# Kernel tuning notes

Hardware: AMD Instinct MI355X
Metric: run time of the kernel (lower is better)

The kernel has to match this reference:

```python
import jax, jax.numpy as jnp
import numpy as np

SEQ, BS, H, D = 2048, 2, 16, 64


def phi(x):
    # ELU(x / d**0.25) + 1
    return jax.nn.elu(x / (x.shape[-1] ** 0.25)) + 1.0


def setup_inputs() -> dict:
    key = jax.random.key(0)
    ks = jax.random.split(key, 5)
    return {
        "query_layer": jax.random.normal(ks[0], (SEQ, BS, H, D), jnp.float32),
        "key_layer": jax.random.normal(ks[1], (SEQ, BS, H, D), jnp.float32),
        "value_layer": jax.random.normal(ks[2], (SEQ, BS, H, D), jnp.float32),
        "attention_mask": jnp.zeros((BS, 1, SEQ, SEQ), dtype=bool),  # unused by forward
        "phi_k": jax.random.normal(ks[3], (1, H, D, 1), jnp.float32) / 10000.0,
        "phi_kv": jax.random.normal(ks[4], (1, H, D, D), jnp.float32) / 10000.0,
    }


def _ntk_attn(q, k, v, sum_phi_k, sum_phi_kv):
    # q,k,v: [bs,h,n,d]; sum_phi_k: [1,h,d,1]; sum_phi_kv: [1,h,d,d]
    d = q.shape[-1]
    nq, nk = q.shape[-2], k.shape[-2]
    kk = jnp.abs(sum_phi_k)
    Z = sum_phi_kv
    phi_q = phi(q)  # [bs,h,nq,d]
    A = jnp.einsum("bhqd,bhkd->bhqk", q, k) / jnp.sqrt(jnp.float32(d))
    max_A = jnp.max(A, axis=-1, keepdims=True)  # [bs,h,nq,1]
    exp_max_A = jnp.exp(max_A)
    A = jnp.exp(A - max_A)
    causal = jnp.tril(jnp.ones((nq, nk), jnp.float32), k=nk - nq)
    A = A * causal  # broadcast over [bs,h]
    D_norm = jnp.sum(A, axis=-1, keepdims=True) + jnp.matmul(phi_q, kk) / exp_max_A
    ctx = (jnp.matmul(A, v) + jnp.matmul(phi_q, Z) / exp_max_A) / D_norm
    return ctx  # [bs,h,nq,d]


def reference(query_layer, key_layer, value_layer, attention_mask, phi_k, phi_kv):
    # inputs are [seq, bs, h, d]; attention_mask is unused (module ignores it)
    q = jnp.transpose(query_layer, (1, 2, 0, 3)).astype(jnp.float32)
    k = jnp.transpose(key_layer, (1, 2, 0, 3)).astype(jnp.float32)
    v = jnp.transpose(value_layer, (1, 2, 0, 3)).astype(jnp.float32)
    ctx = _ntk_attn(q, k, v, phi_k, phi_kv)  # [bs,h,nq,d]
    ctx = jnp.transpose(ctx, (2, 0, 1, 3))  # [nq,bs,h,d]
    nq, bs, h, d = ctx.shape
    return ctx.reshape(nq, bs, h * d).astype(query_layer.dtype)
```

## Files before the change

### kernel.cpp

```cpp
#include <hip/hip_runtime.h>

#define SEQ 2048
#define BSZ 2
#define NHEAD 16
#define NBH (BSZ * NHEAD)
#define HDIM 64
#define QBLK 64
#define KVBLK 64
#define NQT (SEQ / QBLK)
#define ROWSTRIDE (BSZ * NHEAD * HDIM)

typedef __bf16 bf16x8 __attribute__((ext_vector_type(8)));
typedef __bf16 bf16x4 __attribute__((ext_vector_type(4)));
typedef float f32x4 __attribute__((ext_vector_type(4)));

#define AS1 __attribute__((address_space(1)))
#define AS3 __attribute__((address_space(3)))

__global__ __launch_bounds__(256)
void conv_k(const float* __restrict__ Kg, __bf16* __restrict__ Kb) {
  const int t = blockIdx.x * 256 + threadIdx.x;
  const int s = t >> 8;
  const int bh = (t >> 3) & 31;
  const int d8 = (t & 7) * 8;
  const float* src = Kg + (size_t)s * ROWSTRIDE + bh * HDIM + d8;
  const float4 a = *(const float4*)src;
  const float4 b = *(const float4*)(src + 4);
  bf16x8 o = {(__bf16)a.x, (__bf16)a.y, (__bf16)a.z, (__bf16)a.w,
              (__bf16)b.x, (__bf16)b.y, (__bf16)b.z, (__bf16)b.w};
  const int slot = (d8 >> 3) ^ (s & 7);
  *(bf16x8*)(Kb + ((size_t)bh * SEQ + s) * HDIM + slot * 8) = o;
}

__global__ __launch_bounds__(256)
void conv_v(const float* __restrict__ Vg, __bf16* __restrict__ Vt) {
  __shared__ __bf16 tt[HDIM][72];
  const int kb = blockIdx.x;
  const int bh = blockIdx.y;
  const int tid = threadIdx.x;
  {
    const int r = tid >> 2, c16 = (tid & 3) * 16;
#pragma unroll
    for (int i = 0; i < 4; ++i) {
      const float4 v = *(const float4*)(Vg + (size_t)(kb * 64 + r) * ROWSTRIDE +
                                        bh * HDIM + c16 + 4 * i);
      tt[c16 + 4 * i + 0][r] = (__bf16)v.x;
      tt[c16 + 4 * i + 1][r] = (__bf16)v.y;
      tt[c16 + 4 * i + 2][r] = (__bf16)v.z;
      tt[c16 + 4 * i + 3][r] = (__bf16)v.w;
    }
  }
  __syncthreads();
  {
    const int d = tid >> 2, c2 = (tid & 3) * 2;
#pragma unroll
    for (int k8 = 0; k8 < 2; ++k8) {
      const int s8 = c2 + k8;
      const int pbase = (s8 ^ (d & 7)) * 8;
      __bf16 ov[8];
#pragma unroll
      for (int j = 0; j < 8; ++j) {
        const int p = pbase + j;
        const int P = p >> 5, g = (p >> 3) & 3, jj = p & 7;
        ov[j] = tt[d][32 * P + 16 * (jj >> 2) + 4 * g + (jj & 3)];
      }
      *(bf16x8*)(Vt + (((size_t)bh * 32 + kb) * 64 + d) * 64 + s8 * 8) =
          *(const bf16x8*)ov;
    }
  }
}

__global__ __launch_bounds__(256)
void conv_z(const float* __restrict__ PKVg, __bf16* __restrict__ Ztb) {
  const int t = blockIdx.x * 256 + threadIdx.x;
  const int lr = t & 15, lg = (t >> 4) & 3, c = (t >> 6) & 1;
  const int dj = (t >> 7) & 3, h = t >> 9;
  __bf16 o[8];
#pragma unroll
  for (int i = 0; i < 8; ++i)
    o[i] = (__bf16)PKVg[((size_t)h * 64 + 32 * c + 8 * lg + i) * 64 + dj * 16 + lr];
  *(bf16x8*)(Ztb + (size_t)t * 8) = *(const bf16x8*)o;
}

__global__ __launch_bounds__(256, 4)
void ntk_attn(const float* __restrict__ Qg, const __bf16* __restrict__ Kb,
              const __bf16* __restrict__ Vt, const float* __restrict__ PKg,
              const __bf16* __restrict__ Ztb, float* __restrict__ Og) {
  __shared__ __bf16 Ks[2][KVBLK * HDIM];
  __shared__ __bf16 Vts[2][KVBLK * HDIM];

  const int tid = threadIdx.x;
  const int w = tid >> 6, l = tid & 63, lr = l & 15, lg = l >> 4;

  const int ord = blockIdx.x;
  const int bh = ord & 31, h = bh & (NHEAD - 1);
  const int v = ord >> 5;
  const int bx = (v < 16) ? v : 47 - v;
  const int q0 = bx * QBLK;
  const int ntile = bx + 1;
  const int headoff = bh * HDIM;
  const __bf16* Kbh = Kb + (size_t)bh * SEQ * HDIM;
  const __bf16* Vbh = Vt + (size_t)bh * SEQ * HDIM;

  auto stage = [&](int kb, int bb) {
    const char* gk = (const char*)Kbh + ((size_t)kb << 13) + (w << 11) + (l << 4);
    const char* gv = (const char*)Vbh + ((size_t)kb << 13) + (w << 11) + (l << 4);
    __bf16* lk = &Ks[bb][w << 10];
    __bf16* lv = &Vts[bb][w << 10];
    __builtin_amdgcn_global_load_lds((const AS1 unsigned*)gk,
                                     (AS3 unsigned*)lk, 16, 0, 0);
    __builtin_amdgcn_global_load_lds((const AS1 unsigned*)(gk + 1024),
                                     (AS3 unsigned*)(lk + 512), 16, 0, 0);
    __builtin_amdgcn_global_load_lds((const AS1 unsigned*)gv,
                                     (AS3 unsigned*)lv, 16, 0, 0);
    __builtin_amdgcn_global_load_lds((const AS1 unsigned*)(gv + 1024),
                                     (AS3 unsigned*)(lv + 512), 16, 0, 0);
  };

  stage(0, 0);

  bf16x8 aq[2], pq[2];
  {
    const float* qp = Qg + (size_t)(q0 + w * 16 + lr) * ROWSTRIDE + headoff + lg * 8;
#pragma unroll
    for (int c = 0; c < 2; ++c) {
      const float4 x0 = *(const float4*)(qp + 32 * c);
      const float4 x1 = *(const float4*)(qp + 32 * c + 4);
      const float f[8] = {x0.x, x0.y, x0.z, x0.w, x1.x, x1.y, x1.z, x1.w};
#pragma unroll
      for (int i = 0; i < 8; ++i) {
        aq[c][i] = (__bf16)(f[i] * 0.125f);
        const float xs = f[i] * 0.3535533905932738f;
        pq[c][i] = (__bf16)(xs > 0.f ? xs + 1.f : __expf(xs));
      }
    }
  }

  const f32x4 z4 = {0.f, 0.f, 0.f, 0.f};
  f32x4 oacc[4] = {z4, z4, z4, z4};
  float lsum = 0.f;
  const int qa = q0 + w * 16 + lr;
  const int sw = lr & 7;

  __syncthreads();
  int cur = 0;

  for (int kb = 0; kb < ntile; ++kb) {
    const bool more = (kb + 1 < ntile);
    if (more) stage(kb + 1, cur ^ 1);

    bf16x8 kc[4][2];
#pragma unroll
    for (int nj = 0; nj < 4; ++nj)
#pragma unroll
      for (int c = 0; c < 2; ++c)
        kc[nj][c] = *(const bf16x8*)&Ks[cur][(nj * 16 + lr) * 64 +
                                            (((4 * c + lg) ^ sw) << 3)];
    bf16x8 vv[2][4];
#pragma unroll
    for (int P = 0; P < 2; ++P)
#pragma unroll
      for (int dj = 0; dj < 4; ++dj)
        vv[P][dj] = *(const bf16x8*)&Vts[cur][(dj * 16 + lr) * 64 +
                                             (((4 * P + lg) ^ sw) << 3)];

    f32x4 s4[4];
    __builtin_amdgcn_s_setprio(1);
#pragma unroll
    for (int nj = 0; nj < 4; ++nj) {
      f32x4 acc = z4;
#pragma unroll
      for (int c = 0; c < 2; ++c)
        acc = __builtin_amdgcn_mfma_f32_16x16x32_bf16(kc[nj][c], aq[c], acc, 0, 0, 0);
      s4[nj] = acc;
    }
    __builtin_amdgcn_s_setprio(0);

    bf16x4 p4[4];
    const bool diag = (kb == bx);
    const int kv0 = kb * KVBLK;
#pragma unroll
    for (int nj = 0; nj < 4; ++nj) {
#pragma unroll
      for (int r = 0; r < 4; ++r) {
        float e;
        if (diag) {
          const int kabs = kv0 + 16 * nj + 4 * lg + r;
          e = (kabs <= qa) ? __expf(s4[nj][r]) : 0.f;
        } else {
          e = __expf(s4[nj][r]);
        }
        lsum += e;
        p4[nj][r] = (__bf16)e;
      }
    }

    __builtin_amdgcn_s_setprio(1);
#pragma unroll
    for (int P = 0; P < 2; ++P) {
      const bf16x8 pa = __builtin_shufflevector(p4[2 * P], p4[2 * P + 1],
                                                0, 1, 2, 3, 4, 5, 6, 7);
#pragma unroll
      for (int dj = 0; dj < 4; ++dj)
        oacc[dj] = __builtin_amdgcn_mfma_f32_16x16x32_bf16(pa, vv[P][dj],
                                                           oacc[dj], 0, 0, 0);
    }
    __builtin_amdgcn_s_setprio(0);

    if (more) {
      __syncthreads();
      cur ^= 1;
    }
  }

  float den;
  {
    float pkk = 0.f;
#pragma unroll
    for (int c = 0; c < 2; ++c) {
      const float* kp = PKg + h * HDIM + 32 * c + 8 * lg;
      const float4 a = *(const float4*)kp;
      const float4 b = *(const float4*)(kp + 4);
      const float ka[8] = {a.x, a.y, a.z, a.w, b.x, b.y, b.z, b.w};
#pragma unroll
      for (int i = 0; i < 8; ++i)
        pkk += (float)pq[c][i] * fabsf(ka[i]);
    }
    pkk += __shfl_xor(pkk, 16);
    pkk += __shfl_xor(pkk, 32);
    float s = lsum;
    s += __shfl_xor(s, 16);
    s += __shfl_xor(s, 32);
    den = s + pkk;
  }

  f32x4 zacc[4] = {z4, z4, z4, z4};
  const __bf16* Zf = Ztb + (size_t)h * 4096;
  __builtin_amdgcn_s_setprio(1);
#pragma unroll
  for (int c = 0; c < 2; ++c) {
#pragma unroll
    for (int dj = 0; dj < 4; ++dj) {
      const bf16x8 bz = *(const bf16x8*)(Zf + ((dj * 2 + c) * 64 + l) * 8);
      zacc[dj] = __builtin_amdgcn_mfma_f32_16x16x32_bf16(pq[c], bz, zacc[dj], 0, 0, 0);
    }
  }
  __builtin_amdgcn_s_setprio(0);

#pragma unroll
  for (int r = 0; r < 4; ++r) {
    const float rd = 1.f / __shfl(den, lg * 4 + r);
    float* op = Og + (size_t)(q0 + w * 16 + lg * 4 + r) * ROWSTRIDE + headoff;
#pragma unroll
    for (int dj = 0; dj < 4; ++dj)
      op[dj * 16 + lr] = (oacc[dj][r] + zacc[dj][r]) * rd;
  }
}

extern "C" void kernel_launch(void* const* d_in, const int* in_sizes, int n_in,
                              void* d_out, int out_size, void* d_ws, size_t ws_size,
                              hipStream_t stream) {
  const float* Qg  = (const float*)d_in[0];
  const float* Kg  = (const float*)d_in[1];
  const float* Vg  = (const float*)d_in[2];
  const float* PKg  = (const float*)d_in[4];
  const float* PKVg = (const float*)d_in[5];
  float* Og = (float*)d_out;

  __bf16* Kb  = (__bf16*)d_ws;
  __bf16* Vt  = Kb + (size_t)NBH * SEQ * HDIM;
  __bf16* Ztb = Vt + (size_t)NBH * SEQ * HDIM;

  conv_k<<<dim3(SEQ * NBH * 8 / 256), dim3(256), 0, stream>>>(Kg, Kb);
  conv_v<<<dim3(SEQ / 64, NBH), dim3(256), 0, stream>>>(Vg, Vt);
  conv_z<<<dim3(32), dim3(256), 0, stream>>>(PKVg, Ztb);
  ntk_attn<<<dim3(NQT * NBH), dim3(256), 0, stream>>>(Qg, Kb, Vt, PKg, Ztb, Og);
}
```

Measured before the change: 53.00 us.

## Share K/V tiles across 128-row query blocks, fuse conversion kernels, use exp2

The attention kernel now processes 128 query rows per block with 512 threads, so each staged K/V tile in LDS serves twice as many query rows and global K/V traffic per query row is halved. Waves in the lower half skip the final K tile, which lies entirely above their causal diagonal. The three bf16 conversion kernels are merged into one launch that dispatches on block index, cutting launch overhead. The softmax exponent uses the hardware exp2 with log2(e) folded into the Q scale. In exchange the grid has half as many blocks, which lowers occupancy and parallelism, and some waves sit idle on the last tile.

```diff
diff --git a/kernel.cpp b/kernel.cpp
--- a/kernel.cpp
+++ b/kernel.cpp
@@ -5,7 +5,7 @@
 #define NHEAD 16
 #define NBH (BSZ * NHEAD)
 #define HDIM 64
-#define QBLK 64
+#define QBLK 128
 #define KVBLK 64
 #define NQT (SEQ / QBLK)
 #define ROWSTRIDE (BSZ * NHEAD * HDIM)
@@ -18,71 +18,71 @@
 #define AS3 __attribute__((address_space(3)))
 
 __global__ __launch_bounds__(256)
-void conv_k(const float* __restrict__ Kg, __bf16* __restrict__ Kb) {
-  const int t = blockIdx.x * 256 + threadIdx.x;
-  const int s = t >> 8;
-  const int bh = (t >> 3) & 31;
-  const int d8 = (t & 7) * 8;
-  const float* src = Kg + (size_t)s * ROWSTRIDE + bh * HDIM + d8;
-  const float4 a = *(const float4*)src;
-  const float4 b = *(const float4*)(src + 4);
-  bf16x8 o = {(__bf16)a.x, (__bf16)a.y, (__bf16)a.z, (__bf16)a.w,
-              (__bf16)b.x, (__bf16)b.y, (__bf16)b.z, (__bf16)b.w};
-  const int slot = (d8 >> 3) ^ (s & 7);
-  *(bf16x8*)(Kb + ((size_t)bh * SEQ + s) * HDIM + slot * 8) = o;
+void conv_all(const float* __restrict__ Kg, const float* __restrict__ Vg,
+              const float* __restrict__ PKVg, __bf16* __restrict__ Kb,
+              __bf16* __restrict__ Vt, __bf16* __restrict__ Ztb) {
+  __shared__ __bf16 tt[HDIM][72];
+  const int b = blockIdx.x;
+  const int tid = threadIdx.x;
+
+  if (b < 2048) {
+    const int t = b * 256 + tid;
+    const int s = t >> 8;
+    const int bh = (t >> 3) & 31;
+    const int d8 = (t & 7) * 8;
+    const float* src = Kg + (size_t)s * ROWSTRIDE + bh * HDIM + d8;
+    const float4 a = *(const float4*)src;
+    const float4 bb = *(const float4*)(src + 4);
+    bf16x8 o = {(__bf16)a.x, (__bf16)a.y, (__bf16)a.z, (__bf16)a.w,
+                (__bf16)bb.x, (__bf16)bb.y, (__bf16)bb.z, (__bf16)bb.w};
+    const int slot = (d8 >> 3) ^ (s & 7);
+    *(bf16x8*)(Kb + ((size_t)bh * SEQ + s) * HDIM + slot * 8) = o;
+  } else if (b < 3072) {
+    const int t = b - 2048;
+    const int kb = t & 31, bh = t >> 5;
+    {
+      const int r = tid >> 2, c16 = (tid & 3) * 16;
+#pragma unroll
+      for (int i = 0; i < 4; ++i) {
+        const float4 v = *(const float4*)(Vg + (size_t)(kb * 64 + r) * ROWSTRIDE +
+                                          bh * HDIM + c16 + 4 * i);
+        tt[c16 + 4 * i + 0][r] = (__bf16)v.x;
+        tt[c16 + 4 * i + 1][r] = (__bf16)v.y;
+        tt[c16 + 4 * i + 2][r] = (__bf16)v.z;
+        tt[c16 + 4 * i + 3][r] = (__bf16)v.w;
+      }
+    }
+    __syncthreads();
+    {
+      const int d = tid >> 2, c2 = (tid & 3) * 2;
+#pragma unroll
+      for (int k8 = 0; k8 < 2; ++k8) {
+        const int s8 = c2 + k8;
+        const int pbase = (s8 ^ (d & 7)) * 8;
+        __bf16 ov[8];
+#pragma unroll
+        for (int j = 0; j < 8; ++j) {
+          const int p = pbase + j;
+          const int P = p >> 5, g = (p >> 3) & 3, jj = p & 7;
+          ov[j] = tt[d][32 * P + 16 * (jj >> 2) + 4 * g + (jj & 3)];
+        }
+        *(bf16x8*)(Vt + (((size_t)bh * 32 + kb) * 64 + d) * 64 + s8 * 8) =
+            *(const bf16x8*)ov;
+      }
+    }
+  } else {
+    const int t = (b - 3072) * 256 + tid;
+    const int lr = t & 15, lg = (t >> 4) & 3, c = (t >> 6) & 1;
+    const int dj = (t >> 7) & 3, h = t >> 9;
+    __bf16 o[8];
+#pragma unroll
+    for (int i = 0; i < 8; ++i)
+      o[i] = (__bf16)PKVg[((size_t)h * 64 + 32 * c + 8 * lg + i) * 64 + dj * 16 + lr];
+    *(bf16x8*)(Ztb + (size_t)t * 8) = *(const bf16x8*)o;
+  }
 }
 
-__global__ __launch_bounds__(256)
-void conv_v(const float* __restrict__ Vg, __bf16* __restrict__ Vt) {
-  __shared__ __bf16 tt[HDIM][72];
-  const int kb = blockIdx.x;
-  const int bh = blockIdx.y;
-  const int tid = threadIdx.x;
-  {
-    const int r = tid >> 2, c16 = (tid & 3) * 16;
-#pragma unroll
-    for (int i = 0; i < 4; ++i) {
-      const float4 v = *(const float4*)(Vg + (size_t)(kb * 64 + r) * ROWSTRIDE +
-                                        bh * HDIM + c16 + 4 * i);
-      tt[c16 + 4 * i + 0][r] = (__bf16)v.x;
-      tt[c16 + 4 * i + 1][r] = (__bf16)v.y;
-      tt[c16 + 4 * i + 2][r] = (__bf16)v.z;
-      tt[c16 + 4 * i + 3][r] = (__bf16)v.w;
-    }
-  }
-  __syncthreads();
-  {
-    const int d = tid >> 2, c2 = (tid & 3) * 2;
-#pragma unroll
-    for (int k8 = 0; k8 < 2; ++k8) {
-      const int s8 = c2 + k8;
-      const int pbase = (s8 ^ (d & 7)) * 8;
-      __bf16 ov[8];
-#pragma unroll
-      for (int j = 0; j < 8; ++j) {
-        const int p = pbase + j;
-        const int P = p >> 5, g = (p >> 3) & 3, jj = p & 7;
-        ov[j] = tt[d][32 * P + 16 * (jj >> 2) + 4 * g + (jj & 3)];
-      }
-      *(bf16x8*)(Vt + (((size_t)bh * 32 + kb) * 64 + d) * 64 + s8 * 8) =
-          *(const bf16x8*)ov;
-    }
-  }
-}
-
-__global__ __launch_bounds__(256)
-void conv_z(const float* __restrict__ PKVg, __bf16* __restrict__ Ztb) {
-  const int t = blockIdx.x * 256 + threadIdx.x;
-  const int lr = t & 15, lg = (t >> 4) & 3, c = (t >> 6) & 1;
-  const int dj = (t >> 7) & 3, h = t >> 9;
-  __bf16 o[8];
-#pragma unroll
-  for (int i = 0; i < 8; ++i)
-    o[i] = (__bf16)PKVg[((size_t)h * 64 + 32 * c + 8 * lg + i) * 64 + dj * 16 + lr];
-  *(bf16x8*)(Ztb + (size_t)t * 8) = *(const bf16x8*)o;
-}
-
-__global__ __launch_bounds__(256, 4)
+__global__ __launch_bounds__(512, 4)
 void ntk_attn(const float* __restrict__ Qg, const __bf16* __restrict__ Kb,
               const __bf16* __restrict__ Vt, const float* __restrict__ PKg,
               const __bf16* __restrict__ Ztb, float* __restrict__ Og) {
@@ -95,33 +95,29 @@
   const int ord = blockIdx.x;
   const int bh = ord & 31, h = bh & (NHEAD - 1);
   const int v = ord >> 5;
-  const int bx = (v < 16) ? v : 47 - v;
+  const int bx = (v < 8) ? v : 23 - v;
   const int q0 = bx * QBLK;
-  const int ntile = bx + 1;
+  const int ntile = 2 * bx + 2;
+  const int diagTile = 2 * bx + (w >> 2);
   const int headoff = bh * HDIM;
   const __bf16* Kbh = Kb + (size_t)bh * SEQ * HDIM;
   const __bf16* Vbh = Vt + (size_t)bh * SEQ * HDIM;
 
   auto stage = [&](int kb, int bb) {
-    const char* gk = (const char*)Kbh + ((size_t)kb << 13) + (w << 11) + (l << 4);
-    const char* gv = (const char*)Vbh + ((size_t)kb << 13) + (w << 11) + (l << 4);
-    __bf16* lk = &Ks[bb][w << 10];
-    __bf16* lv = &Vts[bb][w << 10];
+    const char* gk = (const char*)Kbh + ((size_t)kb << 13) + (w << 10) + (l << 4);
+    const char* gv = (const char*)Vbh + ((size_t)kb << 13) + (w << 10) + (l << 4);
     __builtin_amdgcn_global_load_lds((const AS1 unsigned*)gk,
-                                     (AS3 unsigned*)lk, 16, 0, 0);
-    __builtin_amdgcn_global_load_lds((const AS1 unsigned*)(gk + 1024),
-                                     (AS3 unsigned*)(lk + 512), 16, 0, 0);
+                                     (AS3 unsigned*)&Ks[bb][w << 9], 16, 0, 0);
     __builtin_amdgcn_global_load_lds((const AS1 unsigned*)gv,
-                                     (AS3 unsigned*)lv, 16, 0, 0);
-    __builtin_amdgcn_global_load_lds((const AS1 unsigned*)(gv + 1024),
-                                     (AS3 unsigned*)(lv + 512), 16, 0, 0);
+                                     (AS3 unsigned*)&Vts[bb][w << 9], 16, 0, 0);
   };
 
   stage(0, 0);
 
   bf16x8 aq[2], pq[2];
   {
-    const float* qp = Qg + (size_t)(q0 + w * 16 + lr) * ROWSTRIDE + headoff + lg * 8;
+    const int qrow = q0 + 64 * (w >> 2) + (w & 3) * 16 + lr;
+    const float* qp = Qg + (size_t)qrow * ROWSTRIDE + headoff + lg * 8;
 #pragma unroll
     for (int c = 0; c < 2; ++c) {
       const float4 x0 = *(const float4*)(qp + 32 * c);
@@ -129,7 +125,7 @@
       const float f[8] = {x0.x, x0.y, x0.z, x0.w, x1.x, x1.y, x1.z, x1.w};
 #pragma unroll
       for (int i = 0; i < 8; ++i) {
-        aq[c][i] = (__bf16)(f[i] * 0.125f);
+        aq[c][i] = (__bf16)(f[i] * 0.18033688011112042f);
         const float xs = f[i] * 0.3535533905932738f;
         pq[c][i] = (__bf16)(xs > 0.f ? xs + 1.f : __expf(xs));
       }
@@ -139,7 +135,7 @@
   const f32x4 z4 = {0.f, 0.f, 0.f, 0.f};
   f32x4 oacc[4] = {z4, z4, z4, z4};
   float lsum = 0.f;
-  const int qa = q0 + w * 16 + lr;
+  const int qa = q0 + 64 * (w >> 2) + (w & 3) * 16 + lr;
   const int sw = lr & 7;
 
   __syncthreads();
@@ -149,63 +145,65 @@
     const bool more = (kb + 1 < ntile);
     if (more) stage(kb + 1, cur ^ 1);
 
-    bf16x8 kc[4][2];
-#pragma unroll
-    for (int nj = 0; nj < 4; ++nj)
-#pragma unroll
-      for (int c = 0; c < 2; ++c)
-        kc[nj][c] = *(const bf16x8*)&Ks[cur][(nj * 16 + lr) * 64 +
-                                            (((4 * c + lg) ^ sw) << 3)];
-    bf16x8 vv[2][4];
-#pragma unroll
-    for (int P = 0; P < 2; ++P)
-#pragma unroll
-      for (int dj = 0; dj < 4; ++dj)
-        vv[P][dj] = *(const bf16x8*)&Vts[cur][(dj * 16 + lr) * 64 +
-                                             (((4 * P + lg) ^ sw) << 3)];
-
-    f32x4 s4[4];
-    __builtin_amdgcn_s_setprio(1);
-#pragma unroll
-    for (int nj = 0; nj < 4; ++nj) {
-      f32x4 acc = z4;
-#pragma unroll
-      for (int c = 0; c < 2; ++c)
-        acc = __builtin_amdgcn_mfma_f32_16x16x32_bf16(kc[nj][c], aq[c], acc, 0, 0, 0);
-      s4[nj] = acc;
-    }
-    __builtin_amdgcn_s_setprio(0);
-
-    bf16x4 p4[4];
-    const bool diag = (kb == bx);
-    const int kv0 = kb * KVBLK;
-#pragma unroll
-    for (int nj = 0; nj < 4; ++nj) {
-#pragma unroll
-      for (int r = 0; r < 4; ++r) {
-        float e;
-        if (diag) {
-          const int kabs = kv0 + 16 * nj + 4 * lg + r;
-          e = (kabs <= qa) ? __expf(s4[nj][r]) : 0.f;
-        } else {
-          e = __expf(s4[nj][r]);
+    if (kb <= diagTile) {
+      bf16x8 kc[4][2];
+#pragma unroll
+      for (int nj = 0; nj < 4; ++nj)
+#pragma unroll
+        for (int c = 0; c < 2; ++c)
+          kc[nj][c] = *(const bf16x8*)&Ks[cur][(nj * 16 + lr) * 64 +
+                                              (((4 * c + lg) ^ sw) << 3)];
+      bf16x8 vv[2][4];
+#pragma unroll
+      for (int P = 0; P < 2; ++P)
+#pragma unroll
+        for (int dj = 0; dj < 4; ++dj)
+          vv[P][dj] = *(const bf16x8*)&Vts[cur][(dj * 16 + lr) * 64 +
+                                               (((4 * P + lg) ^ sw) << 3)];
+
+      f32x4 s4[4];
+      __builtin_amdgcn_s_setprio(1);
+#pragma unroll
+      for (int nj = 0; nj < 4; ++nj) {
+        f32x4 acc = z4;
+#pragma unroll
+        for (int c = 0; c < 2; ++c)
+          acc = __builtin_amdgcn_mfma_f32_16x16x32_bf16(kc[nj][c], aq[c], acc, 0, 0, 0);
+        s4[nj] = acc;
+      }
+      __builtin_amdgcn_s_setprio(0);
+
+      bf16x4 p4[4];
+      const bool diag = (kb == diagTile);
+      const int kv0 = kb * KVBLK;
+#pragma unroll
+      for (int nj = 0; nj < 4; ++nj) {
+#pragma unroll
+        for (int r = 0; r < 4; ++r) {
+          float e;
+          if (diag) {
+            const int kabs = kv0 + 16 * nj + 4 * lg + r;
+            e = (kabs <= qa) ? __builtin_amdgcn_exp2f(s4[nj][r]) : 0.f;
+          } else {
+            e = __builtin_amdgcn_exp2f(s4[nj][r]);
+          }
+          lsum += e;
+          p4[nj][r] = (__bf16)e;
         }
-        lsum += e;
-        p4[nj][r] = (__bf16)e;
-      }
-    }
-
-    __builtin_amdgcn_s_setprio(1);
-#pragma unroll
-    for (int P = 0; P < 2; ++P) {
-      const bf16x8 pa = __builtin_shufflevector(p4[2 * P], p4[2 * P + 1],
-                                                0, 1, 2, 3, 4, 5, 6, 7);
-#pragma unroll
-      for (int dj = 0; dj < 4; ++dj)
-        oacc[dj] = __builtin_amdgcn_mfma_f32_16x16x32_bf16(pa, vv[P][dj],
-                                                           oacc[dj], 0, 0, 0);
-    }
-    __builtin_amdgcn_s_setprio(0);
+      }
+
+      __builtin_amdgcn_s_setprio(1);
+#pragma unroll
+      for (int P = 0; P < 2; ++P) {
+        const bf16x8 pa = __builtin_shufflevector(p4[2 * P], p4[2 * P + 1],
+                                                  0, 1, 2, 3, 4, 5, 6, 7);
+#pragma unroll
+        for (int dj = 0; dj < 4; ++dj)
+          oacc[dj] = __builtin_amdgcn_mfma_f32_16x16x32_bf16(pa, vv[P][dj],
+                                                             oacc[dj], 0, 0, 0);
+      }
+      __builtin_amdgcn_s_setprio(0);
+    }
 
     if (more) {
       __syncthreads();
@@ -250,7 +248,8 @@
 #pragma unroll
   for (int r = 0; r < 4; ++r) {
     const float rd = 1.f / __shfl(den, lg * 4 + r);
-    float* op = Og + (size_t)(q0 + w * 16 + lg * 4 + r) * ROWSTRIDE + headoff;
+    const int qrow = q0 + 64 * (w >> 2) + (w & 3) * 16 + lg * 4 + r;
+    float* op = Og + (size_t)qrow * ROWSTRIDE + headoff;
 #pragma unroll
     for (int dj = 0; dj < 4; ++dj)
       op[dj * 16 + lr] = (oacc[dj][r] + zacc[dj][r]) * rd;
@@ -271,8 +270,7 @@
   __bf16* Vt  = Kb + (size_t)NBH * SEQ * HDIM;
   __bf16* Ztb = Vt + (size_t)NBH * SEQ * HDIM;
 
-  conv_k<<<dim3(SEQ * NBH * 8 / 256), dim3(256), 0, stream>>>(Kg, Kb);
-  conv_v<<<dim3(SEQ / 64, NBH), dim3(256), 0, stream>>>(Vg, Vt);
-  conv_z<<<dim3(32), dim3(256), 0, stream>>>(PKVg, Ztb);
-  ntk_attn<<<dim3(NQT * NBH), dim3(256), 0, stream>>>(Qg, Kb, Vt, PKg, Ztb, Og);
+  conv_all<<<dim3(2048 + 1024 + 32), dim3(256), 0, stream>>>(Kg, Vg, PKVg,
+                                                             Kb, Vt, Ztb);
+  ntk_attn<<<dim3(NQT * NBH), dim3(512), 0, stream>>>(Qg, Kb, Vt, PKg, Ztb, Og);
 }
```

Measured after the change: 51.46 us. 1.03x faster.
